# Performance work log

Measured on AMD Instinct MI355X. Metric: run time of the kernel, lower is better.

Reference implementation:

```python
import jax, jax.numpy as jnp
import numpy as np
from jax import lax

ROI = 7          # roi_size
STRIDE = 16      # stride_prod
MH = MW = 24     # max crop height/width (fixed-size dynamic_slice window)


def setup_inputs() -> dict:
    key = jax.random.key(0)
    ks = jax.random.split(key, 12)
    N, C, Hf, Wf = 128, 512, 38, 38
    x = jax.random.normal(ks[0], (N, C, Hf, Wf), dtype=jnp.float32)
    # region_projs rows are (r, c, w, h): crop is x[:, c:c+h, r:r+w]
    r = jax.random.randint(ks[1], (N,), 0, 15)
    c = jax.random.randint(ks[2], (N,), 0, 15)
    w = jax.random.randint(ks[3], (N,), 4, MW + 1)
    h = jax.random.randint(ks[4], (N,), 4, MH + 1)
    region_projs = jnp.stack([r, c, w, h], axis=1).astype(jnp.int32)
    W1 = jax.random.normal(ks[5], (ROI * ROI * C, 4096), dtype=jnp.float32) * 0.01
    b1 = jnp.zeros((4096,), dtype=jnp.float32)
    W2 = jax.random.normal(ks[6], (4096, 4096), dtype=jnp.float32) * 0.01
    b2 = jnp.zeros((4096,), dtype=jnp.float32)
    Wcls = jax.random.normal(ks[7], (4096, 21), dtype=jnp.float32) * 0.01
    Wbox = jax.random.normal(ks[8], (4096, 80), dtype=jnp.float32) * 0.001
    return {"x": x, "region_projs": region_projs, "W1": W1, "b1": b1,
            "W2": W2, "b2": b2, "Wcls": Wcls, "Wbox": Wbox}


def _roi_adaptive_maxpool(crops, w, h):
    """crops: [N,C,MH,MW]; w,h: [N] int (valid extent). AdaptiveMaxPool2d((7,7)) per ROI."""
    ii = jnp.arange(ROI)
    ys = jnp.arange(MH)
    xs = jnp.arange(MW)
    # adaptive pool bin i of length L covers [floor(i*L/7), ceil((i+1)*L/7))
    rstart = (ii[None, :] * h[:, None]) // ROI            # [N,7]
    rend = ((ii[None, :] + 1) * h[:, None] + ROI - 1) // ROI
    cstart = (ii[None, :] * w[:, None]) // ROI
    cend = ((ii[None, :] + 1) * w[:, None] + ROI - 1) // ROI
    rmask = (ys[None, None, :] >= rstart[:, :, None]) & (ys[None, None, :] < rend[:, :, None])  # [N,7,MH]
    cmask = (xs[None, None, :] >= cstart[:, :, None]) & (xs[None, None, :] < cend[:, :, None])  # [N,7,MW]
    neg = jnp.float32(-jnp.inf)
    rows = [jnp.max(jnp.where(rmask[:, i, None, :, None], crops, neg), axis=2) for i in range(ROI)]
    tmp = jnp.stack(rows, axis=2)  # [N,C,7,MW]
    cols = [jnp.max(jnp.where(cmask[:, j, None, None, :], tmp, neg), axis=3) for j in range(ROI)]
    return jnp.stack(cols, axis=3)  # [N,C,7,7]


def reference(x, region_projs, W1, b1, W2, b2, Wcls, Wbox):
    N, C = x.shape[0], x.shape[1]
    # per-ROI crop: x[idx, :, c:c+h, r:r+w]; fixed-size window, bins mask the valid extent
    crops = jax.vmap(
        lambda xi, b: lax.dynamic_slice(xi, (0, b[1], b[0]), (C, MH, MW))
    )(x, region_projs)  # [N,C,MH,MW]
    pooled = _roi_adaptive_maxpool(crops, region_projs[:, 2], region_projs[:, 3])
    flat = pooled.reshape(N, -1)  # [N, 25088]
    # classifier (Dropout in eval mode = identity)
    h1 = jax.nn.relu(flat @ W1 + b1)
    h2 = jax.nn.relu(h1 @ W2 + b2)
    clf_scores = jax.nn.softmax(h2 @ Wcls, axis=1)          # [N,21]
    bbox_targets = h2 @ Wbox                                 # [N,80]
    # bbox_target_to_pred_bbox, vectorized over rois and classes
    bf = region_projs.astype(jnp.float32)
    r, c, w, h = bf[:, 0:1], bf[:, 1:2], bf[:, 2:3], bf[:, 3:4]  # [N,1]
    t = bbox_targets.reshape(N, 20, 4)
    p0 = jnp.ceil((w * t[..., 0] + r) * STRIDE) - 1.0
    p1 = jnp.ceil((h * t[..., 1] + c) * STRIDE) - 1.0
    p2 = jnp.floor(w * jnp.exp(t[..., 2]) * STRIDE) + 1.0
    p3 = jnp.floor(h * jnp.exp(t[..., 3]) * STRIDE) + 1.0
    bbox_pred = jnp.stack([p0, p1, p2, p3], axis=-1).reshape(N, 80)
    bbox_pred = lax.stop_gradient(bbox_pred)  # torch path detaches via math.ceil/floor
    return clf_scores, bbox_pred
```

## Files before the change

### kernel.cpp

```cpp
#include <hip/hip_runtime.h>
#include <hip/hip_bf16.h>
#include <math.h>

#define N_BATCH 128
#define C_CH    512
#define HF      38
#define WF      38
#define K1      25088
#define NH      4096
#define NCLS    21
#define NBOX    80
#define STEPS1  784
#define STEPS2  128

typedef __attribute__((ext_vector_type(8))) short s16x8;
typedef __attribute__((ext_vector_type(4))) float f32x4;

__device__ __forceinline__ unsigned short bf_rne(float x) {
  unsigned u = __float_as_uint(x);
  return (unsigned short)((u + 0x7FFFu + ((u >> 16) & 1u)) >> 16);
}

__device__ __forceinline__ void gload16(const void* g, void* l) {
  __builtin_amdgcn_global_load_lds(
      (const __attribute__((address_space(1))) unsigned int*)g,
      (__attribute__((address_space(3))) unsigned int*)l, 16, 0, 0);
}

__global__ __launch_bounds__(256) void pool_kernel(
    const float* __restrict__ x, const int* __restrict__ rp,
    unsigned short* __restrict__ Asw) {
  const int n = blockIdx.y, cb = blockIdx.x, tid = threadIdx.x;
  const int r = rp[n*4+0], c = rp[n*4+1], w = rp[n*4+2], h = rp[n*4+3];
  __shared__ float tile[8][24][25];
  __shared__ float pout[392];
  const int ch = tid >> 5, l32 = tid & 31;
  const float* xc = x + (((size_t)(n*C_CH + cb*8 + ch))*HF + c)*WF + r;
  for (int y = 0; y < h; ++y)
    for (int xx = l32; xx < w; xx += 32)
      tile[ch][y][xx] = xc[y*WF + xx];
  __syncthreads();
  for (int o = tid; o < 8*49; o += 256) {
    int ch2 = o / 49, ij = o - ch2*49, i = ij / 7, j = ij - i*7;
    int rs = (i*h)/7, re = ((i+1)*h + 6)/7;
    int cs = (j*w)/7, ce = ((j+1)*w + 6)/7;
    float m = -INFINITY;
    for (int y = rs; y < re; ++y)
      for (int xx = cs; xx < ce; ++xx)
        m = fmaxf(m, tile[ch2][y][xx]);
    pout[o] = m;
  }
  __syncthreads();
  if (tid < 49) {
    const int mt = n >> 4, mlo = n & 15;
    const int kl0 = tid * 8;
    const int kg0 = cb*392 + kl0;
    const int S = kg0 >> 5, kg = (kg0 >> 3) & 3;
    size_t base = ((size_t)S*8 + mt)*512 + (size_t)(kg*16 + mlo)*8;
    unsigned short q[8];
    #pragma unroll
    for (int e = 0; e < 8; ++e) q[e] = bf_rne(pout[kl0 + e]);
    ushort4 lo; lo.x=q[0]; lo.y=q[1]; lo.z=q[2]; lo.w=q[3];
    ushort4 hi; hi.x=q[4]; hi.y=q[5]; hi.z=q[6]; hi.w=q[7];
    *(ushort4*)(Asw + base)     = lo;
    *(ushort4*)(Asw + base + 4) = hi;
  }
}

__global__ __launch_bounds__(256, 3) void gemm_v17(
    const unsigned short* __restrict__ Asw, const float* __restrict__ B,
    float* __restrict__ part, const int nsteps, const int swz) {
  __shared__ char smem[49152];
  const int tid = threadIdx.x, lane = tid & 63, wv = tid >> 6;
  const int wr = wv >> 1, wc = wv & 1;
  const int bid = blockIdx.x;
  int nb, ks;
  if (swz) {
    const int xcd = bid & 7, j = bid >> 3;
    nb = j & 31;
    ks = xcd*2 + (j >> 5);
  } else {
    nb = bid & 31;
    ks = bid >> 5;
  }
  const int l15 = lane & 15, lq = lane >> 4;
  const float* Bg0 = B + (size_t)nb * 128;

  f32x4 acc[4][4];
  #pragma unroll
  for (int i = 0; i < 4; ++i)
    #pragma unroll
    for (int j2 = 0; j2 < 4; ++j2) acc[i][j2] = (f32x4){0.f, 0.f, 0.f, 0.f};

#define STAGE(s, bufb) do { \
    char* Ad = smem + (bufb); \
    char* Bd = smem + (bufb) + 8192; \
    _Pragma("unroll") \
    for (int t_ = 0; t_ < 6; ++t_) { \
      const int i_ = wv*6 + t_; \
      if (i_ < 8) { \
        gload16((const char*)Asw + (((size_t)(ks*nsteps + (s))*8 + i_) << 10) \
                    + lane*16, \
                Ad + (i_ << 10)); \
      } else { \
        const int j_ = i_ - 8; \
        const int row_ = 2*j_ + (lane >> 5); \
        const int gc_ = ((lane & 31)*4) ^ (8*((row_ >> 3) & 3)); \
        gload16(Bg0 + ((size_t)(ks*nsteps + (s))*32 + row_)*NH + gc_, \
                Bd + (j_ << 10)); \
      } \
    } } while (0)

  STAGE(0, 0);
  __syncthreads();

  int bufb = 0;
  for (int s = 0; s < nsteps; ++s) {
    if (s + 1 < nsteps) STAGE(s + 1, bufb ^ 24576);
    const char* Ab = smem + bufb;
    const float* Bf = (const float*)(smem + bufb + 8192);
    s16x8 bf0[4];
    #pragma unroll
    for (int nt = 0; nt < 4; ++nt) {
      #pragma unroll
      for (int e = 0; e < 8; ++e) {
        float xv = Bf[(lq*8 + e)*128 + ((wc*64 + nt*16 + l15) ^ (8*lq))];
        bf0[nt][e] = (short)bf_rne(xv);
      }
    }
    #pragma unroll
    for (int ml = 0; ml < 4; ++ml) {
      const s16x8 a0 = *(const s16x8*)(Ab + ((wr*4 + ml) << 10) + lane*16);
      #pragma unroll
      for (int nt = 0; nt < 4; ++nt)
        acc[ml][nt] = __builtin_amdgcn_mfma_f32_16x16x32_bf16(
            a0, bf0[nt], acc[ml][nt], 0, 0, 0);
    }
    __syncthreads();
    bufb ^= 24576;
  }
#undef STAGE
  float* Pb = part + (size_t)ks*N_BATCH*NH + (size_t)nb*128 + wc*64;
  #pragma unroll
  for (int ml = 0; ml < 4; ++ml)
    #pragma unroll
    for (int nt = 0; nt < 4; ++nt)
      #pragma unroll
      for (int rr = 0; rr < 4; ++rr)
        Pb[(size_t)((wr*4 + ml)*16 + lq*4 + rr)*NH + nt*16 + l15]
            = acc[ml][nt][rr];
}

__global__ __launch_bounds__(256) void reduce_k(
    const float* __restrict__ part, const float* __restrict__ bias,
    unsigned short* __restrict__ AswOut, float* __restrict__ f32out,
    int KS, int mode) {
  const int idx = blockIdx.x*256 + threadIdx.x;
  float4 s = ((const float4*)part)[idx];
  for (int k2 = 1; k2 < KS; ++k2) {
    float4 p = ((const float4*)part)[(size_t)k2*131072 + idx];
    s.x += p.x; s.y += p.y; s.z += p.z; s.w += p.w;
  }
  float4 bv = ((const float4*)bias)[idx & 1023];
  float v[4];
  v[0] = fmaxf(s.x + bv.x, 0.f); v[1] = fmaxf(s.y + bv.y, 0.f);
  v[2] = fmaxf(s.z + bv.z, 0.f); v[3] = fmaxf(s.w + bv.w, 0.f);
  if (mode == 1) {
    float4 o; o.x = v[0]; o.y = v[1]; o.z = v[2]; o.w = v[3];
    ((float4*)f32out)[idx] = o;
  } else {
    int m = idx >> 10, k = (idx & 1023) * 4;
    int S = k >> 5, kg = (k >> 3) & 3, e0 = k & 7;
    size_t base = ((size_t)S*8 + (m >> 4))*512
                + (size_t)(kg*16 + (m & 15))*8 + e0;
    ushort4 st;
    st.x = bf_rne(v[0]); st.y = bf_rne(v[1]);
    st.z = bf_rne(v[2]); st.w = bf_rne(v[3]);
    *(ushort4*)(AswOut + base) = st;
  }
}

__global__ __launch_bounds__(256) void head_transpose(
    const float* __restrict__ Wcls, const float* __restrict__ Wbox,
    float* __restrict__ WT) {
  const int c = blockIdx.x;
  const float* src; int stride;
  if (c < NCLS) { src = Wcls + c; stride = NCLS; }
  else          { src = Wbox + (c - NCLS); stride = NBOX; }
  for (int k = threadIdx.x; k < NH; k += 256)
    WT[(size_t)c*NH + k] = src[(size_t)k*stride];
}

__global__ __launch_bounds__(512) void head_fused(
    const float* __restrict__ h2, const float* __restrict__ WT,
    const int* __restrict__ rp, float* __restrict__ out) {
  const int n = blockIdx.x, tid = threadIdx.x;
  const int wv = tid >> 6, lane = tid & 63;
  __shared__ float h2s[NH];
  __shared__ float dots[104];
  __shared__ float red[2];
  for (int i = tid; i < NH/4; i += 512)
    ((float4*)h2s)[i] = ((const float4*)(h2 + (size_t)n*NH))[i];
  __syncthreads();
  for (int c = wv; c < NCLS + NBOX; c += 8) {
    const float4* hp = (const float4*)h2s;
    const float4* wp = (const float4*)(WT + (size_t)c*NH);
    float s0=0.f, s1=0.f, s2=0.f, s3=0.f;
    #pragma unroll
    for (int it = 0; it < 16; ++it) {
      float4 a = hp[it*64 + lane];
      float4 b = wp[it*64 + lane];
      s0 = fmaf(a.x, b.x, s0); s1 = fmaf(a.y, b.y, s1);
      s2 = fmaf(a.z, b.z, s2); s3 = fmaf(a.w, b.w, s3);
    }
    float v = (s0 + s1) + (s2 + s3);
    #pragma unroll
    for (int m = 32; m >= 1; m >>= 1) v += __shfl_xor(v, m, 64);
    if (lane == 0) dots[c] = v;
  }
  __syncthreads();
  if (tid == 0) {
    float m = dots[0];
    for (int i = 1; i < NCLS; ++i) m = fmaxf(m, dots[i]);
    float s = 0.f;
    for (int i = 0; i < NCLS; ++i) s += expf(dots[i] - m);
    red[0] = m; red[1] = s;
  }
  __syncthreads();
  if (tid < NCLS) {
    out[(size_t)n*NCLS + tid] = expf(dots[tid] - red[0]) / red[1];
  } else if (tid < NCLS + NBOX) {
    const int j = tid - NCLS;
    const float t  = dots[tid];
    const float rf = (float)rp[n*4+0];
    const float cf = (float)rp[n*4+1];
    const float wf = (float)rp[n*4+2];
    const float hf = (float)rp[n*4+3];
    float p;
    switch (j & 3) {
      case 0:  p = ceilf (__fmul_rn(__fadd_rn(__fmul_rn(wf, t), rf), 16.f)) - 1.f; break;
      case 1:  p = ceilf (__fmul_rn(__fadd_rn(__fmul_rn(hf, t), cf), 16.f)) - 1.f; break;
      case 2:  p = floorf(__fmul_rn(__fmul_rn(wf, expf(t)), 16.f)) + 1.f; break;
      default: p = floorf(__fmul_rn(__fmul_rn(hf, expf(t)), 16.f)) + 1.f; break;
    }
    out[(size_t)N_BATCH*NCLS + (size_t)n*NBOX + j] = p;
  }
}

extern "C" void kernel_launch(void* const* d_in, const int* in_sizes, int n_in,
                              void* d_out, int out_size, void* d_ws, size_t ws_size,
                              hipStream_t stream) {
  const float* x    = (const float*)d_in[0];
  const int*   rp   = (const int*)  d_in[1];
  const float* W1   = (const float*)d_in[2];
  const float* b1   = (const float*)d_in[3];
  const float* W2   = (const float*)d_in[4];
  const float* b2   = (const float*)d_in[5];
  const float* Wcls = (const float*)d_in[6];
  const float* Wbox = (const float*)d_in[7];
  float* out = (float*)d_out;

  char* wp = (char*)d_ws;
  unsigned short* Asw1 = (unsigned short*)wp; wp += (size_t)STEPS1*8192;
  unsigned short* Asw2 = (unsigned short*)wp; wp += (size_t)STEPS2*8192;
  float* h2f = (float*)wp;            wp += (size_t)N_BATCH*NH*4;
  float* WT  = (float*)wp;            wp += (size_t)(NCLS+NBOX)*NH*4;
  float* part = (float*)wp;
  const size_t fixed = (size_t)(wp - (char*)d_ws);
  const size_t slab = (size_t)N_BATCH*NH*4;
  const int KS = 16;
  const int swz = (fixed + 16*slab <= ws_size) ? 1 : 1;

  pool_kernel<<<dim3(64, 128), 256, 0, stream>>>(x, rp, Asw1);
  head_transpose<<<dim3(NCLS + NBOX), 256, 0, stream>>>(Wcls, Wbox, WT);

  gemm_v17<<<dim3(512), 256, 0, stream>>>(Asw1, W1, part, STEPS1/KS, swz);
  reduce_k<<<dim3(512), 256, 0, stream>>>(part, b1, Asw2, nullptr, KS, 0);

  gemm_v17<<<dim3(512), 256, 0, stream>>>(Asw2, W2, part, STEPS2/KS, swz);
  reduce_k<<<dim3(512), 256, 0, stream>>>(part, b2, nullptr, h2f, KS, 1);

  head_fused<<<dim3(128), 512, 0, stream>>>(h2f, WT, rp, out);
}
```

Measured before the change: 242.8 us.

## Load GEMM operands directly from global into registers, dropping LDS staging

```diff
diff --git a/kernel.cpp b/kernel.cpp
--- a/kernel.cpp
+++ b/kernel.cpp
@@ -19,12 +19,6 @@
 __device__ __forceinline__ unsigned short bf_rne(float x) {
   unsigned u = __float_as_uint(x);
   return (unsigned short)((u + 0x7FFFu + ((u >> 16) & 1u)) >> 16);
-}
-
-__device__ __forceinline__ void gload16(const void* g, void* l) {
-  __builtin_amdgcn_global_load_lds(
-      (const __attribute__((address_space(1))) unsigned int*)g,
-      (__attribute__((address_space(3))) unsigned int*)l, 16, 0, 0);
 }
 
 __global__ __launch_bounds__(256) void pool_kernel(
@@ -67,10 +61,9 @@
   }
 }
 
-__global__ __launch_bounds__(256, 3) void gemm_v17(
+__global__ __launch_bounds__(256) void gemm_v18(
     const unsigned short* __restrict__ Asw, const float* __restrict__ B,
     float* __restrict__ part, const int nsteps, const int swz) {
-  __shared__ char smem[49152];
   const int tid = threadIdx.x, lane = tid & 63, wv = tid >> 6;
   const int wr = wv >> 1, wc = wv & 1;
   const int bid = blockIdx.x;
@@ -84,7 +77,9 @@
     ks = bid >> 5;
   }
   const int l15 = lane & 15, lq = lane >> 4;
-  const float* Bg0 = B + (size_t)nb * 128;
+  const unsigned short* Ag = Asw + ((size_t)ks*nsteps*8)*512 + lane*8;
+  const float* Bg = B + ((size_t)ks*nsteps*32 + lq*8)*NH
+                  + (size_t)nb*128 + wc*64 + l15;
 
   f32x4 acc[4][4];
   #pragma unroll
@@ -92,54 +87,32 @@
     #pragma unroll
     for (int j2 = 0; j2 < 4; ++j2) acc[i][j2] = (f32x4){0.f, 0.f, 0.f, 0.f};
 
-#define STAGE(s, bufb) do { \
-    char* Ad = smem + (bufb); \
-    char* Bd = smem + (bufb) + 8192; \
-    _Pragma("unroll") \
-    for (int t_ = 0; t_ < 6; ++t_) { \
-      const int i_ = wv*6 + t_; \
-      if (i_ < 8) { \
-        gload16((const char*)Asw + (((size_t)(ks*nsteps + (s))*8 + i_) << 10) \
-                    + lane*16, \
-                Ad + (i_ << 10)); \
-      } else { \
-        const int j_ = i_ - 8; \
-        const int row_ = 2*j_ + (lane >> 5); \
-        const int gc_ = ((lane & 31)*4) ^ (8*((row_ >> 3) & 3)); \
-        gload16(Bg0 + ((size_t)(ks*nsteps + (s))*32 + row_)*NH + gc_, \
-                Bd + (j_ << 10)); \
-      } \
-    } } while (0)
-
-  STAGE(0, 0);
-  __syncthreads();
-
-  int bufb = 0;
   for (int s = 0; s < nsteps; ++s) {
-    if (s + 1 < nsteps) STAGE(s + 1, bufb ^ 24576);
-    const char* Ab = smem + bufb;
-    const float* Bf = (const float*)(smem + bufb + 8192);
-    s16x8 bf0[4];
-    #pragma unroll
-    for (int nt = 0; nt < 4; ++nt) {
-      #pragma unroll
-      for (int e = 0; e < 8; ++e) {
-        float xv = Bf[(lq*8 + e)*128 + ((wc*64 + nt*16 + l15) ^ (8*lq))];
-        bf0[nt][e] = (short)bf_rne(xv);
-      }
-    }
-    #pragma unroll
-    for (int ml = 0; ml < 4; ++ml) {
-      const s16x8 a0 = *(const s16x8*)(Ab + ((wr*4 + ml) << 10) + lane*16);
+    const float* Bs = Bg + (size_t)s*32*NH;
+    float fB[4][8];
+    #pragma unroll
+    for (int nt = 0; nt < 4; ++nt)
+      #pragma unroll
+      for (int e = 0; e < 8; ++e)
+        fB[nt][e] = Bs[(size_t)e*NH + nt*16];
+    s16x8 bf[4];
+    #pragma unroll
+    for (int nt = 0; nt < 4; ++nt)
+      #pragma unroll
+      for (int e = 0; e < 8; ++e)
+        bf[nt][e] = (short)bf_rne(fB[nt][e]);
+    const unsigned short* As = Ag + (size_t)s*8*512;
+    s16x8 a[4];
+    #pragma unroll
+    for (int ml = 0; ml < 4; ++ml)
+      a[ml] = *(const s16x8*)(As + (size_t)(wr*4 + ml)*512);
+    #pragma unroll
+    for (int ml = 0; ml < 4; ++ml)
       #pragma unroll
       for (int nt = 0; nt < 4; ++nt)
         acc[ml][nt] = __builtin_amdgcn_mfma_f32_16x16x32_bf16(
-            a0, bf0[nt], acc[ml][nt], 0, 0, 0);
-    }
-    __syncthreads();
-    bufb ^= 24576;
-  }
-#undef STAGE
+            a[ml], bf[nt], acc[ml][nt], 0, 0, 0);
+  }
   float* Pb = part + (size_t)ks*N_BATCH*NH + (size_t)nb*128 + wc*64;
   #pragma unroll
   for (int ml = 0; ml < 4; ++ml)
@@ -266,18 +239,16 @@
   float* h2f = (float*)wp;            wp += (size_t)N_BATCH*NH*4;
   float* WT  = (float*)wp;            wp += (size_t)(NCLS+NBOX)*NH*4;
   float* part = (float*)wp;
-  const size_t fixed = (size_t)(wp - (char*)d_ws);
-  const size_t slab = (size_t)N_BATCH*NH*4;
   const int KS = 16;
-  const int swz = (fixed + 16*slab <= ws_size) ? 1 : 1;
+  const int swz = 1;
 
   pool_kernel<<<dim3(64, 128), 256, 0, stream>>>(x, rp, Asw1);
   head_transpose<<<dim3(NCLS + NBOX), 256, 0, stream>>>(Wcls, Wbox, WT);
 
-  gemm_v17<<<dim3(512), 256, 0, stream>>>(Asw1, W1, part, STEPS1/KS, swz);
+  gemm_v18<<<dim3(512), 256, 0, stream>>>(Asw1, W1, part, STEPS1/KS, swz);
   reduce_k<<<dim3(512), 256, 0, stream>>>(part, b1, Asw2, nullptr, KS, 0);
 
-  gemm_v17<<<dim3(512), 256, 0, stream>>>(Asw2, W2, part, STEPS2/KS, swz);
+  gemm_v18<<<dim3(512), 256, 0, stream>>>(Asw2, W2, part, STEPS2/KS, swz);
   reduce_k<<<dim3(512), 256, 0, stream>>>(part, b2, nullptr, h2f, KS, 1);
 
   head_fused<<<dim3(128), 512, 0, stream>>>(h2f, WT, rp, out);
```

Result: slower. 272.7 us (+12.3%).
